# Optimization experiments

Hardware: AMD Instinct MI355X
Metric: run time of the kernel (lower is better)

Reference implementation:

```python
import jax, jax.numpy as jnp
import numpy as np

GRID_SIZE = 5
SPLINE_ORDER = 3
MODES = 16


def make_grid():
    # efficient-kan grid: linspace on [-1,1] extended by spline_order steps each side
    h = 2.0 / GRID_SIZE
    return jnp.arange(-SPLINE_ORDER, GRID_SIZE + SPLINE_ORDER + 1, dtype=jnp.float32) * h - 1.0  # (12,)


def b_splines(x, grid):
    # x: (N, d) -> (N, d, GRID_SIZE + SPLINE_ORDER) via Cox-de Boor recursion
    xe = x[..., None]
    bases = ((xe >= grid[:-1]) & (xe < grid[1:])).astype(x.dtype)
    for k in range(1, SPLINE_ORDER + 1):
        left = (xe - grid[: -(k + 1)]) / (grid[k:-1] - grid[: -(k + 1)])
        right = (grid[k + 1:] - xe) / (grid[k + 1:] - grid[1:-k])
        bases = left * bases[..., :-1] + right * bases[..., 1:]
    return bases


def kan_linear(x, base_w, spline_w, scaler, grid):
    # base branch: silu(x) @ W_b^T ; spline branch: B(x) contracted with scaled coeffs
    base = jax.nn.silu(x) @ base_w.T
    b = b_splines(x, grid)  # (N, in, K)
    spline = jnp.einsum('nik,oik->no', b, spline_w * scaler[..., None])
    return base + spline


def spectral_conv2d(x, w1, w2):
    # x: (b, c, h, w) real; w1/w2: (c_in, c_out, MODES, MODES) complex
    b, c, h, w = x.shape
    x_ft = jnp.fft.rfft2(x)  # (b, c, h, w//2+1)
    out_ft = jnp.zeros((b, c, h, w // 2 + 1), dtype=jnp.complex64)
    out_ft = out_ft.at[:, :, :MODES, :MODES].set(
        jnp.einsum('bixy,ioxy->boxy', x_ft[:, :, :MODES, :MODES], w1))
    out_ft = out_ft.at[:, :, -MODES:, :MODES].set(
        jnp.einsum('bixy,ioxy->boxy', x_ft[:, :, -MODES:, :MODES], w2))
    return jnp.fft.irfft2(out_ft, s=(h, w))


def setup_inputs() -> dict:
    key = jax.random.key(0)
    ks = jax.random.split(key, 13)
    c = 64
    sc = 1.0 / c  # FNO-style scale
    inp = {
        'x': jax.random.normal(ks[0], (16, c, 128, 128), dtype=jnp.float32),
        'spec_w1_r': jax.random.normal(ks[1], (c, c, MODES, MODES), dtype=jnp.float32) * sc,
        'spec_w1_i': jax.random.normal(ks[2], (c, c, MODES, MODES), dtype=jnp.float32) * sc,
        'spec_w2_r': jax.random.normal(ks[3], (c, c, MODES, MODES), dtype=jnp.float32) * sc,
        'spec_w2_i': jax.random.normal(ks[4], (c, c, MODES, MODES), dtype=jnp.float32) * sc,
        'conv_w': jax.random.normal(ks[5], (c, c), dtype=jnp.float32) * 0.05,
        'conv_b': jax.random.normal(ks[6], (c,), dtype=jnp.float32) * 0.05,
        'k1_base': jax.random.normal(ks[7], (c, c), dtype=jnp.float32) * 0.05,
        'k1_spline': jax.random.normal(ks[8], (c, c, GRID_SIZE + SPLINE_ORDER), dtype=jnp.float32) * 0.05,
        'k1_scaler': jax.random.normal(ks[9], (c, c), dtype=jnp.float32) * 0.05 + 1.0,
        'k2_base': jax.random.normal(ks[10], (c, c), dtype=jnp.float32) * 0.05,
        'k2_spline': jax.random.normal(ks[11], (c, c, GRID_SIZE + SPLINE_ORDER), dtype=jnp.float32) * 0.05,
        'k2_scaler': jax.random.normal(ks[12], (c, c), dtype=jnp.float32) * 0.05 + 1.0,
    }
    return inp


def reference(x, spec_w1_r, spec_w1_i, spec_w2_r, spec_w2_i, conv_w, conv_b,
              k1_base, k1_spline, k1_scaler, k2_base, k2_spline, k2_scaler):
    grid = make_grid()
    w1 = spec_w1_r + 1j * spec_w1_i
    w2 = spec_w2_r + 1j * spec_w2_i
    x1 = spectral_conv2d(x, w1, w2)
    x2 = jnp.einsum('bchw,oc->bohw', x, conv_w) + conv_b[None, :, None, None]
    y = x1 + x2
    b, c, h, w = y.shape
    y_flat = y.transpose(0, 2, 3, 1).reshape(-1, c)  # (b*h*w, c)
    y_flat = kan_linear(y_flat, k1_base, k1_spline, k1_scaler, grid)
    y_flat = kan_linear(y_flat, k2_base, k2_spline, k2_scaler, grid)
    y = y_flat.reshape(b, h, w, c).transpose(0, 3, 1, 2)
    return jax.nn.gelu(y, approximate=False)
```

## Files before the change

### kernel.cpp

```cpp
#include <hip/hip_runtime.h>


typedef _Float16 half8 __attribute__((ext_vector_type(8)));
typedef float f32x4 __attribute__((ext_vector_type(4)));
typedef unsigned u32x2 __attribute__((ext_vector_type(2)));
typedef unsigned u32x4 __attribute__((ext_vector_type(4)));
typedef unsigned long long u64;

#define ROWB 1168
#define ROWX 144

__device__ __forceinline__ unsigned pk2(float a, float b) {
  auto h = __builtin_amdgcn_cvt_pkrtz(a, b);
  return __builtin_bit_cast(unsigned, h);
}

__global__ __launch_bounds__(256) void prep_dft_tables_kernel(
    half8* __restrict__ T1f, half8* __restrict__ A2c, half8* __restrict__ A2s,
    half8* __restrict__ A2sn, half8* __restrict__ A3c, half8* __restrict__ A3s,
    half8* __restrict__ A3sn) {
  int idx = blockIdx.x * 256 + threadIdx.x;
  if (idx >= 7 * 512) return;
  int tab = idx >> 9, e = idx & 511, l = e & 63, eg = e >> 6;
  int lg = l >> 4, li = l & 15;
  const double W0 = 6.283185307179586476925287 / 128.0;
  half8 hv;
#pragma unroll
  for (int j = 0; j < 8; ++j) {
    float val;
    if (tab == 0) {
      int ks = eg >> 1, nt = eg & 1;
      int w = ks * 32 + lg * 8 + j, kx = li;
      int t = (w * kx) & 127;
      float s, c;
      sincosf((float)((double)t * W0), &s, &c);
      val = nt ? -s : c;
    } else if (tab <= 3) {
      int mt = eg >> 2, ks = eg & 3;
      int mp = mt * 16 + li;
      int ky = mp < 16 ? mp : mp + 96;
      int h = ks * 32 + lg * 8 + j;
      int t = (ky * h) & 127;
      float s, c;
      sincosf((float)((double)t * W0), &s, &c);
      val = (tab == 1) ? c : (tab == 2) ? s : -s;
    } else {
      int h = eg * 16 + li;
      int m = lg * 8 + j;
      int ky = m < 16 ? m : m + 96;
      int t = (ky * h) & 127;
      float s, c;
      sincosf((float)((double)t * W0), &s, &c);
      val = (tab == 4) ? c : (tab == 5) ? s : -s;
    }
    hv[j] = (_Float16)val;
  }
  half8* dst = (tab == 0)   ? T1f
               : (tab == 1) ? A2c
               : (tab == 2) ? A2s
               : (tab == 3) ? A2sn
               : (tab == 4) ? A3c
               : (tab == 5) ? A3s
                            : A3sn;
  dst[e] = hv;
}

__global__ __launch_bounds__(256) void fwd_dft_kernel(
    const float* __restrict__ x, float* __restrict__ XfRe, float* __restrict__ XfIm,
    const half8* __restrict__ T1f, const half8* __restrict__ A2c,
    const half8* __restrict__ A2s, const half8* __restrict__ A2sn) {
  __shared__ __align__(16) char sImg[128 * 272];
  __shared__ __align__(16) char sXw[32 * 272];
  const int tid = threadIdx.x;
  const int l = tid & 63, wv = tid >> 6;
  const int rit = l & 15, g = l >> 4;
  const int bc = blockIdx.x;
  const float4* src4 = (const float4*)(x + (size_t)bc * 16384);

  half8 t1f[8];
#pragma unroll
  for (int i = 0; i < 8; ++i) t1f[i] = T1f[i * 64 + l];
  const int mt2 = wv & 1, nt2 = wv >> 1;
  const half8* a2op = (nt2 == 0) ? A2s : A2sn;
  half8 a2c[4], a2o[4];
#pragma unroll
  for (int ks = 0; ks < 4; ++ks) {
    a2c[ks] = A2c[(mt2 * 4 + ks) * 64 + l];
    a2o[ks] = a2op[(mt2 * 4 + ks) * 64 + l];
  }

#pragma unroll
  for (int i = 0; i < 16; ++i) {
    int idx = i * 256 + tid;
    int r = idx >> 5, c4 = idx & 31;
    float4 v = src4[idx];
    u32x2 p = {pk2(v.x, v.y), pk2(v.z, v.w)};
    *(u32x2*)(sImg + r * 272 + c4 * 8) = p;
  }
  __syncthreads();

  const f32x4 z = {0.f, 0.f, 0.f, 0.f};
  f32x4 s1[2][2];
  s1[0][0] = z; s1[0][1] = z; s1[1][0] = z; s1[1][1] = z;
#pragma unroll
  for (int ks = 0; ks < 4; ++ks) {
#pragma unroll
    for (int mi = 0; mi < 2; ++mi) {
      const char* pa = sImg + ((wv * 2 + mi) * 16 + rit) * 272 + ks * 64 + g * 16;
      half8 a = *(const half8*)pa;
      s1[mi][0] = __builtin_amdgcn_mfma_f32_16x16x32_f16(a, t1f[ks * 2 + 0], s1[mi][0], 0, 0, 0);
      s1[mi][1] = __builtin_amdgcn_mfma_f32_16x16x32_f16(a, t1f[ks * 2 + 1], s1[mi][1], 0, 0, 0);
    }
  }
#pragma unroll
  for (int mi = 0; mi < 2; ++mi)
#pragma unroll
    for (int nt = 0; nt < 2; ++nt) {
      u32x2 p = {pk2(s1[mi][nt][0], s1[mi][nt][1]), pk2(s1[mi][nt][2], s1[mi][nt][3])};
      *(u32x2*)(sXw + (nt * 16 + rit) * 272 + ((wv * 2 + mi) * 16 + g * 4) * 2) = p;
    }
  __syncthreads();

  f32x4 acc2 = z;
#pragma unroll
  for (int ks = 0; ks < 4; ++ks) {
    half8 bre = *(const half8*)(sXw + rit * 272 + ks * 64 + g * 16);
    half8 bim = *(const half8*)(sXw + (16 + rit) * 272 + ks * 64 + g * 16);
    half8 b1 = (nt2 == 0) ? bre : bim;
    half8 b2 = (nt2 == 0) ? bim : bre;
    acc2 = __builtin_amdgcn_mfma_f32_16x16x32_f16(a2c[ks], b1, acc2, 0, 0, 0);
    acc2 = __builtin_amdgcn_mfma_f32_16x16x32_f16(a2o[ks], b2, acc2, 0, 0, 0);
  }
  float* outp = ((nt2 == 0) ? XfRe : XfIm) + (size_t)bc * 512 + (mt2 * 16 + g * 4) * 16 + rit;
#pragma unroll
  for (int r = 0; r < 4; ++r) outp[r * 16] = acc2[r];
}

__global__ __launch_bounds__(256) void mode_mix_kernel(
    float* __restrict__ XfRe, float* __restrict__ XfIm,
    const float* __restrict__ w1r, const float* __restrict__ w1i,
    const float* __restrict__ w2r, const float* __restrict__ w2i) {
  __shared__ float Wr[4096];
  __shared__ float Wi[4096];
  __shared__ float Ar[1024];
  __shared__ float Ai[1024];
  const int tid = threadIdx.x;
  const int bid = blockIdx.x;
  const int mode = ((bid & 7) << 6) | (bid >> 3);
  const int m = mode >> 4, kx = mode & 15;
  const float* wr = (m < 16) ? w1r : w2r;
  const float* wi = (m < 16) ? w1i : w2i;
  const int woff = (m & 15) * 16 + kx;
  for (int e = tid; e < 4096; e += 256) {
    Wr[e] = wr[(size_t)e * 256 + woff];
    Wi[e] = wi[(size_t)e * 256 + woff];
  }
  for (int e = tid; e < 1024; e += 256) {
    Ar[e] = XfRe[(size_t)e * 512 + mode];
    Ai[e] = XfIm[(size_t)e * 512 + mode];
  }
  __syncthreads();
  const int o = tid & 63;
  const int b0 = tid >> 6;
  float outR[4], outI[4];
#pragma unroll
  for (int bb = 0; bb < 4; ++bb) {
    const int b = b0 * 4 + bb;
    float re = 0.f, im = 0.f;
    for (int i = 0; i < 64; ++i) {
      float ar = Ar[b * 64 + i], ai = Ai[b * 64 + i];
      float br = Wr[i * 64 + o], bi = Wi[i * 64 + o];
      re += ar * br - ai * bi;
      im += ar * bi + ai * br;
    }
    outR[bb] = re;
    outI[bb] = im;
  }
#pragma unroll
  for (int bb = 0; bb < 4; ++bb) {
    const int b = b0 * 4 + bb;
    size_t off = (size_t)(b * 64 + o) * 512 + mode;
    XfRe[off] = outR[bb];
    XfIm[off] = outI[bb];
  }
}

__global__ __launch_bounds__(256) void inv_h_kernel(
    const float* __restrict__ GfRe, const float* __restrict__ GfIm,
    _Float16* __restrict__ Y1h, const half8* __restrict__ A3c,
    const half8* __restrict__ A3s, const half8* __restrict__ A3sn) {
  __shared__ __align__(16) char Ysh[128 * 80];
  const int tid = threadIdx.x;
  const int l = tid & 63, wv = tid >> 6;
  const int rit = l & 15, g = l >> 4;
  const int bo = blockIdx.x;
  const int bb = bo >> 6, o = bo & 63;
  float gr[8], gi[8];
#pragma unroll
  for (int j = 0; j < 8; ++j) {
    size_t off = (size_t)bo * 512 + (size_t)(g * 8 + j) * 16 + rit;
    gr[j] = GfRe[off];
    gi[j] = GfIm[off];
  }
  u32x4 ur, ui;
#pragma unroll
  for (int p = 0; p < 4; ++p) {
    ur[p] = pk2(gr[2 * p] * 9.765625e-4f, gr[2 * p + 1] * 9.765625e-4f);
    ui[p] = pk2(gi[2 * p] * 9.765625e-4f, gi[2 * p + 1] * 9.765625e-4f);
  }
  half8 grF = __builtin_bit_cast(half8, ur);
  half8 giF = __builtin_bit_cast(half8, ui);
  half8 a3c[2], a3s[2], a3sn[2];
#pragma unroll
  for (int mi = 0; mi < 2; ++mi) {
    a3c[mi] = A3c[(wv * 2 + mi) * 64 + l];
    a3s[mi] = A3s[(wv * 2 + mi) * 64 + l];
    a3sn[mi] = A3sn[(wv * 2 + mi) * 64 + l];
  }
  const f32x4 z = {0.f, 0.f, 0.f, 0.f};
#pragma unroll
  for (int mi = 0; mi < 2; ++mi) {
    f32x4 ar = z, ai = z;
    ar = __builtin_amdgcn_mfma_f32_16x16x32_f16(a3c[mi], grF, ar, 0, 0, 0);
    ar = __builtin_amdgcn_mfma_f32_16x16x32_f16(a3sn[mi], giF, ar, 0, 0, 0);
    ai = __builtin_amdgcn_mfma_f32_16x16x32_f16(a3s[mi], grF, ai, 0, 0, 0);
    ai = __builtin_amdgcn_mfma_f32_16x16x32_f16(a3c[mi], giF, ai, 0, 0, 0);
#pragma unroll
    for (int r = 0; r < 4; ++r) {
      int h = (wv * 2 + mi) * 16 + g * 4 + r;
      *(_Float16*)(Ysh + h * 80 + rit * 2) = (_Float16)ar[r];
      *(_Float16*)(Ysh + h * 80 + (16 + rit) * 2) = (_Float16)ai[r];
    }
  }
  __syncthreads();
#pragma unroll
  for (int i = 0; i < 2; ++i) {
    int idx = i * 256 + tid;
    int h = idx >> 2, q = idx & 3;
    u32x4 v = *(const u32x4*)(Ysh + h * 80 + q * 16);
    *(u32x4*)(Y1h + ((size_t)(bb * 128 + h) * 64 + o) * 32 + q * 8) = v;
  }
}

__global__ __launch_bounds__(256) void prep_bfrag_kernel(
    const float* __restrict__ base_w, const float* __restrict__ spline_w,
    const float* __restrict__ scaler, half8* __restrict__ out) {
  int idx = blockIdx.x * 256 + threadIdx.x;
  if (idx >= 4608) return;
  int lane = idx & 63;
  int ks = (idx >> 6) % 18;
  int nt = idx / (64 * 18);
  int n = nt * 16 + (lane & 15);
  int k0 = ks * 32 + (lane >> 4) * 8;
  half8 hv;
#pragma unroll
  for (int j = 0; j < 8; ++j) {
    int k = k0 + j;
    float val;
    if (k < 64) {
      val = base_w[n * 64 + k];
    } else {
      int c = (k - 64) >> 3, jj = (k - 64) & 7;
      val = spline_w[(n * 64 + c) * 8 + jj] * scaler[n * 64 + c];
    }
    hv[j] = (_Float16)val;
  }
  out[idx] = hv;
}

__global__ __launch_bounds__(256) void prep_conv_kernel(
    const float* __restrict__ convw, half8* __restrict__ Wfrag,
    half8* __restrict__ Tfrag) {
  int idx = blockIdx.x * 256 + threadIdx.x;
  if (idx < 512) {
    int l = idx & 63, ks = (idx >> 6) & 1, nt = idx >> 7;
    int cout = nt * 16 + (l & 15);
    int cin0 = ks * 32 + (l >> 4) * 8;
    half8 hv;
#pragma unroll
    for (int j = 0; j < 8; ++j) hv[j] = (_Float16)convw[cout * 64 + cin0 + j];
    Wfrag[idx] = hv;
  } else if (idx < 1024) {
    int e = idx - 512;
    int w = e >> 2, g = e & 3;
    half8 hv;
#pragma unroll
    for (int j = 0; j < 8; ++j) {
      int k = g * 8 + j;
      float coeff;
      if (k < 16) {
        int t = (k * w) & 127;
        coeff = (k == 0) ? 1.f
                         : 2.f * cosf((float)((double)t * (6.283185307179586476925287 / 128.0)));
      } else {
        int kx = k - 16;
        int t = (kx * w) & 127;
        coeff = (kx == 0) ? 0.f
                          : -2.f * sinf((float)((double)t * (6.283185307179586476925287 / 128.0)));
      }
      hv[j] = (_Float16)(coeff * 0.0625f);
    }
    Tfrag[e] = hv;
  }
}

__device__ __forceinline__ float fast_silu(float v) {
  return v * (1.f / (1.f + __expf(-v)));
}

__device__ __forceinline__ void spline_scatter(char* p16, float v) {
  const float Klo = __fsub_rn(__fmul_rn(-3.f, 0.4f), 1.0f);
  float u = (v - Klo) * 2.5f;
  float uc = fminf(fmaxf(u, 0.f), 10.5f);
  int i = (int)uc;
  float t = u - (float)i;
  float t2 = t * t, t3 = t2 * t;
  float omt = 1.f - t;
  float p0 = t3 * (1.f / 6.f);
  float p3 = omt * omt * (omt * (1.f / 6.f));
  float p1 = fmaf(t3, -0.5f, fmaf(t2, 0.5f, fmaf(t, 0.5f, 1.f / 6.f)));
  float p2 = fmaf(t3, 0.5f, fmaf(t2, -1.f, 2.f / 3.f));
  bool ok = (u >= 0.f) && (u < 11.f);
  unsigned a32 = ok ? pk2(p3, p2) : 0u;
  unsigned b32 = ok ? pk2(p1, p0) : 0u;
  u64 P = ((u64)b32 << 32) | a32;
  int sh = i << 4;
  u64 tA = P >> ((48 - sh) & 63);
  u64 tB = P << ((sh - 48) & 63);
  u64 tC = P >> ((112 - sh) & 63);
  u64 tD = P << ((sh - 112) & 63);
  u64 lo = (sh < 64) ? tA : ((sh < 112) ? tB : 0ull);
  u64 hi = (sh < 64) ? 0ull : ((sh < 128) ? tC : tD);
  u32x4 st = {(unsigned)lo, (unsigned)(lo >> 32), (unsigned)hi, (unsigned)(hi >> 32)};
  *(u32x4*)p16 = st;
}

__device__ __forceinline__ float gelu_exact(float v) {
  return 0.5f * v * (1.f + erff(v * 0.70710678118654752f));
}

__device__ __forceinline__ void w2feat(char* S, int g, int nt, int rit, f32x4 a) {
  const int c = nt * 16 + rit;
#pragma unroll
  for (int r = 0; r < 4; ++r) {
    char* row = S + (g * 4 + r) * ROWB;
    float v = a[r];
    *(_Float16*)(row + c * 2) = (_Float16)fast_silu(v);
    spline_scatter(row + 128 + c * 16, v);
  }
}

__device__ __forceinline__ void gemm_slot_ks(const char* S, const half8* Bq,
                                             int nt, int l, int rit, int g,
                                             f32x4& acc) {
  const half8* bq = Bq + (size_t)nt * 18 * 64 + l;
  const char* pa = S + rit * ROWB + g * 16;
#pragma unroll
  for (int kh = 0; kh < 2; ++kh) {
    half8 bfr[9];
#pragma unroll
    for (int ks = 0; ks < 9; ++ks) bfr[ks] = bq[(kh * 9 + ks) * 64];
#pragma unroll
    for (int ks = 0; ks < 9; ++ks) {
      half8 a = *(const half8*)(pa + (kh * 9 + ks) * 64);
      acc = __builtin_amdgcn_mfma_f32_16x16x32_f16(a, bfr[ks], acc, 0, 0, 0);
    }
  }
}

__device__ __forceinline__ void bounce_acc(float* bnc, int c, int px0, f32x4 a) {
  float* row = bnc + c * 65 + px0;
#pragma unroll
  for (int r = 0; r < 4; ++r) row[r] = gelu_exact(a[r]);
}

__global__ __launch_bounds__(256, 4) void kan_mega_kernel(
    const float* __restrict__ x, float* __restrict__ y,
    const _Float16* __restrict__ Y1h,
    const half8* __restrict__ Bq1, const half8* __restrict__ Bq2,
    const half8* __restrict__ Wfrag, const half8* __restrict__ Tfrag,
    const float* __restrict__ convb) {
  __shared__ __align__(16) char Abuf[2 * 16 * ROWB];
  char* A0 = Abuf;
  char* A1 = Abuf + 16 * ROWB;
  float* ybounce = (float*)A1;
  const int tid = threadIdx.x;
  const int l = tid & 63;
  const int nt = tid >> 6;
  const int rit = l & 15, g = l >> 4;
  const int n0 = blockIdx.x * 64;
  const int b = n0 >> 14;
  const int rem = n0 & 16383;
  const int hrow = rem >> 7, w0 = rem & 127;
  float* base = y + (size_t)b * 1048576 + (size_t)hrow * 128 + w0;
  const float* xbase = x + (size_t)b * 1048576 + (size_t)hrow * 128 + w0;

  half8 By = ((const half8*)Y1h)[((size_t)(b * 128 + hrow) * 64 + nt * 16 + rit) * 4 + g];
  half8 Wf0 = Wfrag[(nt * 2 + 0) * 64 + l];
  half8 Wf1 = Wfrag[(nt * 2 + 1) * 64 + l];
  half8 Tf0 = Tfrag[(w0 + 0 + rit) * 4 + g];
  half8 Tf1 = Tfrag[(w0 + 16 + rit) * 4 + g];
  half8 Tf2 = Tfrag[(w0 + 32 + rit) * 4 + g];
  half8 Tf3 = Tfrag[(w0 + 48 + rit) * 4 + g];
  const float cbv = convb[nt * 16 + rit];

  {
    const int c = tid >> 2, lq = tid & 3;
    const float* bx = xbase + (size_t)c * 16384;
#pragma unroll
    for (int s = 0; s < 4; ++s) {
      float4 v = *(const float4*)(bx + lq * 4 + s * 16);
      const float* vp = (const float*)&v;
#pragma unroll
      for (int j = 0; j < 4; ++j)
        *(_Float16*)(A0 + (lq * 4 + s * 16 + j) * ROWX + c * 2) = (_Float16)vp[j];
    }
  }
  __syncthreads();

  const f32x4 z = {0.f, 0.f, 0.f, 0.f};
  f32x4 a00 = z, a01 = z, a02 = z, a03 = z;
#define CONV_TILE(acc, mt, TF)                                                \
  {                                                                           \
    const char* pa = A0 + (mt * 16 + rit) * ROWX;                             \
    acc = __builtin_amdgcn_mfma_f32_16x16x32_f16(TF, By, z, 0, 0, 0);         \
    half8 xa0 = *(const half8*)(pa + g * 16);                                 \
    acc = __builtin_amdgcn_mfma_f32_16x16x32_f16(xa0, Wf0, acc, 0, 0, 0);     \
    half8 xa1 = *(const half8*)(pa + 64 + g * 16);                            \
    acc = __builtin_amdgcn_mfma_f32_16x16x32_f16(xa1, Wf1, acc, 0, 0, 0);     \
    acc[0] += cbv; acc[1] += cbv; acc[2] += cbv; acc[3] += cbv;               \
  }
  CONV_TILE(a00, 0, Tf0)
  CONV_TILE(a01, 1, Tf1)
  CONV_TILE(a02, 2, Tf2)
  CONV_TILE(a03, 3, Tf3)
#undef CONV_TILE
  w2feat(A1, g, nt, rit, a00);
  __syncthreads();

  f32x4 a10 = z, a11 = z, a12 = z, a13 = z;
  f32x4 a20 = z, a21 = z, a22 = z, a23 = z;
  gemm_slot_ks(A1, Bq1, nt, l, rit, g, a10); w2feat(A0, g, nt, rit, a01);
  __syncthreads();
  gemm_slot_ks(A0, Bq1, nt, l, rit, g, a11); w2feat(A1, g, nt, rit, a02);
  __syncthreads();
  gemm_slot_ks(A1, Bq1, nt, l, rit, g, a12); w2feat(A0, g, nt, rit, a03);
  __syncthreads();
  gemm_slot_ks(A0, Bq1, nt, l, rit, g, a13); w2feat(A1, g, nt, rit, a10);
  __syncthreads();
  gemm_slot_ks(A1, Bq2, nt, l, rit, g, a20); w2feat(A0, g, nt, rit, a11);
  __syncthreads();
  gemm_slot_ks(A0, Bq2, nt, l, rit, g, a21); w2feat(A1, g, nt, rit, a12);
  __syncthreads();
  gemm_slot_ks(A1, Bq2, nt, l, rit, g, a22); w2feat(A0, g, nt, rit, a13);
  __syncthreads();
  const int cch = nt * 16 + rit;
  gemm_slot_ks(A0, Bq2, nt, l, rit, g, a23);
  bounce_acc(ybounce, cch, 0 + g * 4, a20);
  bounce_acc(ybounce, cch, 16 + g * 4, a21);
  bounce_acc(ybounce, cch, 32 + g * 4, a22);
  bounce_acc(ybounce, cch, 48 + g * 4, a23);
  __syncthreads();
#pragma unroll
  for (int i = 0; i < 4; ++i) {
    int idx = i * 256 + tid;
    int c = idx >> 4, q = idx & 15;
    const float* r = ybounce + c * 65 + q * 4;
    float4 v;
    v.x = r[0]; v.y = r[1]; v.z = r[2]; v.w = r[3];
    *(float4*)(base + (size_t)c * 16384 + q * 4) = v;
  }
}

extern "C" void kernel_launch(void* const* d_in, const int* in_sizes, int n_in,
                              void* d_out, int out_size, void* d_ws, size_t ws_size,
                              hipStream_t stream) {
  const float* x    = (const float*)d_in[0];
  const float* w1r  = (const float*)d_in[1];
  const float* w1i  = (const float*)d_in[2];
  const float* w2r  = (const float*)d_in[3];
  const float* w2i  = (const float*)d_in[4];
  const float* cw   = (const float*)d_in[5];
  const float* cb   = (const float*)d_in[6];
  const float* k1b  = (const float*)d_in[7];
  const float* k1s  = (const float*)d_in[8];
  const float* k1sc = (const float*)d_in[9];
  const float* k2b  = (const float*)d_in[10];
  const float* k2s  = (const float*)d_in[11];
  const float* k2sc = (const float*)d_in[12];

  char* ws = (char*)d_ws;
  float*     XfRe  = (float*)(ws + 0);
  float*     XfIm  = (float*)(ws + 2097152);
  _Float16*  Y1h   = (_Float16*)(ws + 4194304);
  half8*     Bf1   = (half8*)(ws + 12582912);
  half8*     Bf2   = (half8*)(ws + 12656640);
  half8*     Wfrag = (half8*)(ws + 12730368);
  half8*     Tfrag = (half8*)(ws + 12738560);
  half8*     T1f   = (half8*)(ws + 12746752);
  half8*     A2c   = (half8*)(ws + 12754944);
  half8*     A2s   = (half8*)(ws + 12763136);
  half8*     A2sn  = (half8*)(ws + 12771328);
  half8*     A3c   = (half8*)(ws + 12779520);
  half8*     A3s   = (half8*)(ws + 12787712);
  half8*     A3sn  = (half8*)(ws + 12795904);
  float* y = (float*)d_out;

  prep_dft_tables_kernel<<<14, 256, 0, stream>>>(T1f, A2c, A2s, A2sn, A3c, A3s, A3sn);
  prep_bfrag_kernel<<<18, 256, 0, stream>>>(k1b, k1s, k1sc, Bf1);
  prep_bfrag_kernel<<<18, 256, 0, stream>>>(k2b, k2s, k2sc, Bf2);
  prep_conv_kernel<<<4, 256, 0, stream>>>(cw, Wfrag, Tfrag);
  fwd_dft_kernel<<<1024, 256, 0, stream>>>(x, XfRe, XfIm, T1f, A2c, A2s, A2sn);
  mode_mix_kernel<<<512, 256, 0, stream>>>(XfRe, XfIm, w1r, w1i, w2r, w2i);
  inv_h_kernel<<<1024, 256, 0, stream>>>(XfRe, XfIm, Y1h, A3c, A3s, A3sn);
  kan_mega_kernel<<<4096, 256, 0, stream>>>(x, y, Y1h, Bf1, Bf2, Wfrag, Tfrag, cb);
}
```

Measured before the change: 174.3 us.

## Merge prep kernels, keep KAN B-fragments in registers, approximate erf in GELU

Four separate prep kernels are merged into one launch to cut launch overhead. In the KAN mega kernel, the 18 B-fragments for each layer are loaded into registers once and reused across the four row slots, instead of being reloaded for every slot. To make room for them, launch bounds drop from 4 to 3 waves. The exact erf in GELU is replaced by the Abramowitz-Stegun polynomial approximation using a fast reciprocal and exp, which lowers accuracy slightly.

```diff
diff --git a/kernel.cpp b/kernel.cpp
--- a/kernel.cpp
+++ b/kernel.cpp
@@ -15,13 +15,11 @@
   return __builtin_bit_cast(unsigned, h);
 }
 
-__global__ __launch_bounds__(256) void prep_dft_tables_kernel(
-    half8* __restrict__ T1f, half8* __restrict__ A2c, half8* __restrict__ A2s,
-    half8* __restrict__ A2sn, half8* __restrict__ A3c, half8* __restrict__ A3s,
-    half8* __restrict__ A3sn) {
-  int idx = blockIdx.x * 256 + threadIdx.x;
-  if (idx >= 7 * 512) return;
-  int tab = idx >> 9, e = idx & 511, l = e & 63, eg = e >> 6;
+__device__ __forceinline__ void prep_dft_elem(int idx7, half8* T1f, half8* A2c,
+                                              half8* A2s, half8* A2sn,
+                                              half8* A3c, half8* A3s,
+                                              half8* A3sn) {
+  int tab = idx7 >> 9, e = idx7 & 511, l = e & 63, eg = e >> 6;
   int lg = l >> 4, li = l & 15;
   const double W0 = 6.283185307179586476925287 / 128.0;
   half8 hv;
@@ -65,6 +63,87 @@
   dst[e] = hv;
 }
 
+__device__ __forceinline__ void prep_bfrag_elem(int idx, const float* base_w,
+                                                const float* spline_w,
+                                                const float* scaler,
+                                                half8* out) {
+  int lane = idx & 63;
+  int ks = (idx >> 6) % 18;
+  int nt = idx / (64 * 18);
+  int n = nt * 16 + (lane & 15);
+  int k0 = ks * 32 + (lane >> 4) * 8;
+  half8 hv;
+#pragma unroll
+  for (int j = 0; j < 8; ++j) {
+    int k = k0 + j;
+    float val;
+    if (k < 64) {
+      val = base_w[n * 64 + k];
+    } else {
+      int c = (k - 64) >> 3, jj = (k - 64) & 7;
+      val = spline_w[(n * 64 + c) * 8 + jj] * scaler[n * 64 + c];
+    }
+    hv[j] = (_Float16)val;
+  }
+  out[idx] = hv;
+}
+
+__device__ __forceinline__ void prep_conv_elem(int idx, const float* convw,
+                                               half8* Wfrag, half8* Tfrag) {
+  if (idx < 512) {
+    int l = idx & 63, ks = (idx >> 6) & 1, nt = idx >> 7;
+    int cout = nt * 16 + (l & 15);
+    int cin0 = ks * 32 + (l >> 4) * 8;
+    half8 hv;
+#pragma unroll
+    for (int j = 0; j < 8; ++j) hv[j] = (_Float16)convw[cout * 64 + cin0 + j];
+    Wfrag[idx] = hv;
+  } else {
+    int e = idx - 512;
+    int w = e >> 2, g = e & 3;
+    half8 hv;
+#pragma unroll
+    for (int j = 0; j < 8; ++j) {
+      int k = g * 8 + j;
+      float coeff;
+      if (k < 16) {
+        int t = (k * w) & 127;
+        coeff = (k == 0) ? 1.f
+                         : 2.f * cosf((float)((double)t * (6.283185307179586476925287 / 128.0)));
+      } else {
+        int kx = k - 16;
+        int t = (kx * w) & 127;
+        coeff = (kx == 0) ? 0.f
+                          : -2.f * sinf((float)((double)t * (6.283185307179586476925287 / 128.0)));
+      }
+      hv[j] = (_Float16)(coeff * 0.0625f);
+    }
+    Tfrag[e] = hv;
+  }
+}
+
+__global__ __launch_bounds__(256) void prep_all_kernel(
+    const float* __restrict__ k1b, const float* __restrict__ k1s,
+    const float* __restrict__ k1sc, const float* __restrict__ k2b,
+    const float* __restrict__ k2s, const float* __restrict__ k2sc,
+    const float* __restrict__ convw,
+    half8* __restrict__ Bf1, half8* __restrict__ Bf2,
+    half8* __restrict__ Wfrag, half8* __restrict__ Tfrag,
+    half8* __restrict__ T1f, half8* __restrict__ A2c, half8* __restrict__ A2s,
+    half8* __restrict__ A2sn, half8* __restrict__ A3c, half8* __restrict__ A3s,
+    half8* __restrict__ A3sn) {
+  int idx = blockIdx.x * 256 + threadIdx.x;
+  if (idx < 3584) {
+    prep_dft_elem(idx, T1f, A2c, A2s, A2sn, A3c, A3s, A3sn);
+  } else if (idx < 8192) {
+    prep_bfrag_elem(idx - 3584, k1b, k1s, k1sc, Bf1);
+  } else if (idx < 12800) {
+    prep_bfrag_elem(idx - 8192, k2b, k2s, k2sc, Bf2);
+  } else if (idx < 13824) {
+    prep_conv_elem(idx - 12800, convw, Wfrag, Tfrag);
+  }
+}
+
 __global__ __launch_bounds__(256) void fwd_dft_kernel(
     const float* __restrict__ x, float* __restrict__ XfRe, float* __restrict__ XfIm,
     const half8* __restrict__ T1f, const half8* __restrict__ A2c,
@@ -239,68 +318,6 @@
     int h = idx >> 2, q = idx & 3;
     u32x4 v = *(const u32x4*)(Ysh + h * 80 + q * 16);
     *(u32x4*)(Y1h + ((size_t)(bb * 128 + h) * 64 + o) * 32 + q * 8) = v;
-  }
-}
-
-__global__ __launch_bounds__(256) void prep_bfrag_kernel(
-    const float* __restrict__ base_w, const float* __restrict__ spline_w,
-    const float* __restrict__ scaler, half8* __restrict__ out) {
-  int idx = blockIdx.x * 256 + threadIdx.x;
-  if (idx >= 4608) return;
-  int lane = idx & 63;
-  int ks = (idx >> 6) % 18;
-  int nt = idx / (64 * 18);
-  int n = nt * 16 + (lane & 15);
-  int k0 = ks * 32 + (lane >> 4) * 8;
-  half8 hv;
-#pragma unroll
-  for (int j = 0; j < 8; ++j) {
-    int k = k0 + j;
-    float val;
-    if (k < 64) {
-      val = base_w[n * 64 + k];
-    } else {
-      int c = (k - 64) >> 3, jj = (k - 64) & 7;
-      val = spline_w[(n * 64 + c) * 8 + jj] * scaler[n * 64 + c];
-    }
-    hv[j] = (_Float16)val;
-  }
-  out[idx] = hv;
-}
-
-__global__ __launch_bounds__(256) void prep_conv_kernel(
-    const float* __restrict__ convw, half8* __restrict__ Wfrag,
-    half8* __restrict__ Tfrag) {
-  int idx = blockIdx.x * 256 + threadIdx.x;
-  if (idx < 512) {
-    int l = idx & 63, ks = (idx >> 6) & 1, nt = idx >> 7;
-    int cout = nt * 16 + (l & 15);
-    int cin0 = ks * 32 + (l >> 4) * 8;
-    half8 hv;
-#pragma unroll
-    for (int j = 0; j < 8; ++j) hv[j] = (_Float16)convw[cout * 64 + cin0 + j];
-    Wfrag[idx] = hv;
-  } else if (idx < 1024) {
-    int e = idx - 512;
-    int w = e >> 2, g = e & 3;
-    half8 hv;
-#pragma unroll
-    for (int j = 0; j < 8; ++j) {
-      int k = g * 8 + j;
-      float coeff;
-      if (k < 16) {
-        int t = (k * w) & 127;
-        coeff = (k == 0) ? 1.f
-                         : 2.f * cosf((float)((double)t * (6.283185307179586476925287 / 128.0)));
-      } else {
-        int kx = k - 16;
-        int t = (kx * w) & 127;
-        coeff = (kx == 0) ? 0.f
-                          : -2.f * sinf((float)((double)t * (6.283185307179586476925287 / 128.0)));
-      }
-      hv[j] = (_Float16)(coeff * 0.0625f);
-    }
-    Tfrag[e] = hv;
   }
 }
 
@@ -336,7 +353,13 @@
 }
 
 __device__ __forceinline__ float gelu_exact(float v) {
-  return 0.5f * v * (1.f + erff(v * 0.70710678118654752f));
+  float x = fabsf(v) * 0.70710678118654752f;
+  float t = __builtin_amdgcn_rcpf(fmaf(0.3275911f, x, 1.0f));
+  float p = fmaf(fmaf(fmaf(fmaf(1.061405429f, t, -1.453152027f), t,
+                           1.421413741f), t, -0.284496736f), t, 0.254829592f) * t;
+  float e = __expf(-x * x);
+  float erfa = fmaf(-p, e, 1.0f);
+  return 0.5f * v * (1.0f + copysignf(erfa, v));
 }
 
 __device__ __forceinline__ void w2feat(char* S, int g, int nt, int rit, f32x4 a) {
@@ -350,21 +373,20 @@
   }
 }
 
-__device__ __forceinline__ void gemm_slot_ks(const char* S, const half8* Bq,
-                                             int nt, int l, int rit, int g,
-                                             f32x4& acc) {
+__device__ __forceinline__ void load_bfrags(half8* B, const half8* Bq, int nt,
+                                            int l) {
   const half8* bq = Bq + (size_t)nt * 18 * 64 + l;
+#pragma unroll
+  for (int ks = 0; ks < 18; ++ks) B[ks] = bq[ks * 64];
+}
+
+__device__ __forceinline__ void gemm_slot_res(const char* S, const half8* B,
+                                              int rit, int g, f32x4& acc) {
   const char* pa = S + rit * ROWB + g * 16;
 #pragma unroll
-  for (int kh = 0; kh < 2; ++kh) {
-    half8 bfr[9];
-#pragma unroll
-    for (int ks = 0; ks < 9; ++ks) bfr[ks] = bq[(kh * 9 + ks) * 64];
-#pragma unroll
-    for (int ks = 0; ks < 9; ++ks) {
-      half8 a = *(const half8*)(pa + (kh * 9 + ks) * 64);
-      acc = __builtin_amdgcn_mfma_f32_16x16x32_f16(a, bfr[ks], acc, 0, 0, 0);
-    }
+  for (int ks = 0; ks < 18; ++ks) {
+    half8 a = *(const half8*)(pa + ks * 64);
+    acc = __builtin_amdgcn_mfma_f32_16x16x32_f16(a, B[ks], acc, 0, 0, 0);
   }
 }
 
@@ -374,7 +396,7 @@
   for (int r = 0; r < 4; ++r) row[r] = gelu_exact(a[r]);
 }
 
-__global__ __launch_bounds__(256, 4) void kan_mega_kernel(
+__global__ __launch_bounds__(256, 3) void kan_mega_kernel(
     const float* __restrict__ x, float* __restrict__ y,
     const _Float16* __restrict__ Y1h,
     const half8* __restrict__ Bq1, const half8* __restrict__ Bq2,
@@ -404,6 +426,9 @@
   half8 Tf3 = Tfrag[(w0 + 48 + rit) * 4 + g];
   const float cbv = convb[nt * 16 + rit];
 
+  half8 B[18];
+  load_bfrags(B, Bq1, nt, l);
+
   {
     const int c = tid >> 2, lq = tid & 3;
     const float* bx = xbase + (size_t)c * 16384;
@@ -440,22 +465,24 @@
 
   f32x4 a10 = z, a11 = z, a12 = z, a13 = z;
   f32x4 a20 = z, a21 = z, a22 = z, a23 = z;
-  gemm_slot_ks(A1, Bq1, nt, l, rit, g, a10); w2feat(A0, g, nt, rit, a01);
-  __syncthreads();
-  gemm_slot_ks(A0, Bq1, nt, l, rit, g, a11); w2feat(A1, g, nt, rit, a02);
-  __syncthreads();
-  gemm_slot_ks(A1, Bq1, nt, l, rit, g, a12); w2feat(A0, g, nt, rit, a03);
-  __syncthreads();
-  gemm_slot_ks(A0, Bq1, nt, l, rit, g, a13); w2feat(A1, g, nt, rit, a10);
-  __syncthreads();
-  gemm_slot_ks(A1, Bq2, nt, l, rit, g, a20); w2feat(A0, g, nt, rit, a11);
-  __syncthreads();
-  gemm_slot_ks(A0, Bq2, nt, l, rit, g, a21); w2feat(A1, g, nt, rit, a12);
-  __syncthreads();
-  gemm_slot_ks(A1, Bq2, nt, l, rit, g, a22); w2feat(A0, g, nt, rit, a13);
+  gemm_slot_res(A1, B, rit, g, a10); w2feat(A0, g, nt, rit, a01);
+  __syncthreads();
+  gemm_slot_res(A0, B, rit, g, a11); w2feat(A1, g, nt, rit, a02);
+  __syncthreads();
+  gemm_slot_res(A1, B, rit, g, a12); w2feat(A0, g, nt, rit, a03);
+  __syncthreads();
+  gemm_slot_res(A0, B, rit, g, a13);
+  load_bfrags(B, Bq2, nt, l);
+  w2feat(A1, g, nt, rit, a10);
+  __syncthreads();
+  gemm_slot_res(A1, B, rit, g, a20); w2feat(A0, g, nt, rit, a11);
+  __syncthreads();
+  gemm_slot_res(A0, B, rit, g, a21); w2feat(A1, g, nt, rit, a12);
+  __syncthreads();
+  gemm_slot_res(A1, B, rit, g, a22); w2feat(A0, g, nt, rit, a13);
   __syncthreads();
   const int cch = nt * 16 + rit;
-  gemm_slot_ks(A0, Bq2, nt, l, rit, g, a23);
+  gemm_slot_res(A0, B, rit, g, a23);
   bounce_acc(ybounce, cch, 0 + g * 4, a20);
   bounce_acc(ybounce, cch, 16 + g * 4, a21);
   bounce_acc(ybounce, cch, 32 + g * 4, a22);
@@ -506,10 +533,9 @@
   half8*     A3sn  = (half8*)(ws + 12795904);
   float* y = (float*)d_out;
 
-  prep_dft_tables_kernel<<<14, 256, 0, stream>>>(T1f, A2c, A2s, A2sn, A3c, A3s, A3sn);
-  prep_bfrag_kernel<<<18, 256, 0, stream>>>(k1b, k1s, k1sc, Bf1);
-  prep_bfrag_kernel<<<18, 256, 0, stream>>>(k2b, k2s, k2sc, Bf2);
-  prep_conv_kernel<<<4, 256, 0, stream>>>(cw, Wfrag, Tfrag);
+  prep_all_kernel<<<54, 256, 0, stream>>>(k1b, k1s, k1sc, k2b, k2s, k2sc, cw,
+                                          Bf1, Bf2, Wfrag, Tfrag, T1f, A2c,
+                                          A2s, A2sn, A3c, A3s, A3sn);
   fwd_dft_kernel<<<1024, 256, 0, stream>>>(x, XfRe, XfIm, T1f, A2c, A2s, A2sn);
   mode_mix_kernel<<<512, 256, 0, stream>>>(XfRe, XfIm, w1r, w1i, w2r, w2i);
   inv_h_kernel<<<1024, 256, 0, stream>>>(XfRe, XfIm, Y1h, A3c, A3s, A3sn);
```

Result: faster. 141.0 us (-19.1%).
